# Kernel tuning notes

Hardware: AMD Instinct MI355X
Metric: run time of the kernel (lower is better)

## Reference

```python
import jax, jax.numpy as jnp
import numpy as np

B, S = 2048, 256
V, E, H, LAT, NL = 4, 8, 64, 3, 2
NT = V + 2          # vocab + start + pad tokens
START = V
TEMP = 1.0


def setup_inputs() -> dict:
    key = jax.random.key(0)
    ks = jax.random.split(key, 32)
    def p(k, shape, scale=0.1):
        return jax.random.normal(k, shape, jnp.float32) * scale
    return {
        "tokens": jax.random.randint(ks[0], (B, S), 0, V),
        "emb": p(ks[1], (NT, E)),
        "enc_Wih0": p(ks[2], (3 * H, E)), "enc_Whh0": p(ks[3], (3 * H, H)),
        "enc_bih0": p(ks[4], (3 * H,)), "enc_bhh0": p(ks[5], (3 * H,)),
        "enc_Wih1": p(ks[6], (3 * H, H)), "enc_Whh1": p(ks[7], (3 * H, H)),
        "enc_bih1": p(ks[8], (3 * H,)), "enc_bhh1": p(ks[9], (3 * H,)),
        "fc_mu_W": p(ks[10], (LAT, H)), "fc_mu_b": p(ks[11], (LAT,)),
        "fc_var_W": p(ks[12], (LAT, H)), "fc_var_b": p(ks[13], (LAT,)),
        "dec_emb": p(ks[14], (NT, H)),
        "proj_W": p(ks[15], (H, LAT)), "proj_b": p(ks[16], (H,)),
        "dec_Wih0": p(ks[17], (3 * H, H)), "dec_Whh0": p(ks[18], (3 * H, H)),
        "dec_bih0": p(ks[19], (3 * H,)), "dec_bhh0": p(ks[20], (3 * H,)),
        "dec_Wih1": p(ks[21], (3 * H, H)), "dec_Whh1": p(ks[22], (3 * H, H)),
        "dec_bih1": p(ks[23], (3 * H,)), "dec_bhh1": p(ks[24], (3 * H,)),
        "head_W": p(ks[25], (V, H)), "head_b": p(ks[26], (V,)),
    }


def gru_cell(h, x, Wih, Whh, bih, bhh):
    # PyTorch GRU gate order: reset, update, new
    gi = x @ Wih.T + bih            # [B, 3H]
    gh = h @ Whh.T + bhh            # [B, 3H]
    ir, iz, ig = jnp.split(gi, 3, axis=-1)
    hr, hz, hg = jnp.split(gh, 3, axis=-1)
    r = jax.nn.sigmoid(ir + hr)
    z = jax.nn.sigmoid(iz + hz)
    n = jnp.tanh(ig + r * hg)
    return (1.0 - z) * n + z * h


def run_gru_layer(x, Wih, Whh, bih, bhh):
    # x: [B, S, D] -> (outputs [B, S, H], final hidden [B, H])
    def step(h, xt):
        h2 = gru_cell(h, xt, Wih, Whh, bih, bhh)
        return h2, h2
    h0 = jnp.zeros((x.shape[0], Whh.shape[1]), x.dtype)
    hT, ys = jax.lax.scan(step, h0, x.transpose(1, 0, 2))
    return ys.transpose(1, 0, 2), hT


def reference(tokens, emb, enc_Wih0, enc_Whh0, enc_bih0, enc_bhh0,
              enc_Wih1, enc_Whh1, enc_bih1, enc_bhh1,
              fc_mu_W, fc_mu_b, fc_var_W, fc_var_b,
              dec_emb, proj_W, proj_b,
              dec_Wih0, dec_Whh0, dec_bih0, dec_bhh0,
              dec_Wih1, dec_Whh1, dec_bih1, dec_bhh1,
              head_W, head_b):
    b, s = tokens.shape
    # ---- encode ----
    x = emb[tokens]                                   # [B, S, E]
    seq, _ = run_gru_layer(x, enc_Wih0, enc_Whh0, enc_bih0, enc_bhh0)
    _, h_last = run_gru_layer(seq, enc_Wih1, enc_Whh1, enc_bih1, enc_bhh1)
    mu = h_last @ fc_mu_W.T + fc_mu_b                 # [B, LAT]
    log_var = h_last @ fc_var_W.T + fc_var_b          # [B, LAT]
    # ---- reparameterize ----
    eps = jax.random.normal(jax.random.key(1), mu.shape, mu.dtype)
    z = eps * jnp.exp(0.5 * log_var) + mu
    hz = z @ proj_W.T + proj_b                        # [B, H]; same init for both layers
    tok0 = jnp.full((b,), START, jnp.int32)
    keys = jax.random.split(jax.random.key(2), s)
    def step(carry, k):
        h0, h1, tok = carry
        xe = dec_emb[tok]                             # [B, H]
        h0n = gru_cell(h0, xe, dec_Wih0, dec_Whh0, dec_bih0, dec_bhh0)
        h1n = gru_cell(h1, h0n, dec_Wih1, dec_Whh1, dec_bih1, dec_bhh1)
        logits = (h1n @ head_W.T + head_b) / TEMP     # [B, V]
        probs = jax.nn.softmax(logits, axis=-1)
        nt = jax.random.categorical(k, logits)        # multinomial sample (detached)
        return (h0n, h1n, nt), probs
    _, probs_seq = jax.lax.scan(step, (hz, hz, tok0), keys)   # [S, B, V]
    recons = probs_seq.transpose(1, 0, 2)[:, :, None, :]      # [B, S, 1, V]
    return recons, tokens, mu, log_var
```

## Files before the change

### kernel.cpp

```cpp
#include <hip/hip_runtime.h>
#include <stdint.h>

typedef unsigned int u32;

#define NB   2048
#define SS   256
#define HH   64
#define VV   4
#define LATD 3
#define NTHR 512

#define TOK_OFF (NB*SS*VV)
#define MU_OFF  (TOK_OFF + NB*SS)
#define LV_OFF  (MU_OFF + NB*LATD)

__device__ __forceinline__ void tf2x32(u32 k0, u32 k1, u32 x0, u32 x1, u32& o0, u32& o1){
  u32 k2 = k0 ^ k1 ^ 0x1BD11BDAu;
  x0 += k0; x1 += k1;
#define TFR(r) { x0 += x1; x1 = (x1<<r)|(x1>>(32-r)); x1 ^= x0; }
  TFR(13) TFR(15) TFR(26) TFR(6)   x0 += k1; x1 += k2 + 1u;
  TFR(17) TFR(29) TFR(16) TFR(24)  x0 += k2; x1 += k0 + 2u;
  TFR(13) TFR(15) TFR(26) TFR(6)   x0 += k0; x1 += k1 + 3u;
  TFR(17) TFR(29) TFR(16) TFR(24)  x0 += k1; x1 += k2 + 4u;
  TFR(13) TFR(15) TFR(26) TFR(6)   x0 += k2; x1 += k0 + 5u;
#undef TFR
  o0 = x0; o1 = x1;
}
__device__ __forceinline__ u32 foldb(u32 k0, u32 k1, u32 i){
  u32 a,b; tf2x32(k0,k1,0u,i,a,b); return a^b;
}
__device__ __forceinline__ float b2u(u32 bits){
  union{u32 i;float f;}c; c.i = (bits>>9) | 0x3f800000u; return c.f - 1.0f;
}
__device__ __forceinline__ float erfinv_f(float x){
  float w = -log1pf(-x*x);
  float p;
  if (w < 5.0f){
    w -= 2.5f;
    p = 2.81022636e-08f;
    p = fmaf(p,w, 3.43273939e-07f);
    p = fmaf(p,w,-3.5233877e-06f);
    p = fmaf(p,w,-4.39150654e-06f);
    p = fmaf(p,w, 0.00021858087f);
    p = fmaf(p,w,-0.00125372503f);
    p = fmaf(p,w,-0.00417768164f);
    p = fmaf(p,w, 0.246640727f);
    p = fmaf(p,w, 1.50140941f);
  } else {
    w = sqrtf(w) - 3.0f;
    p = -0.000200214257f;
    p = fmaf(p,w, 0.000100950558f);
    p = fmaf(p,w, 0.00134934322f);
    p = fmaf(p,w,-0.00367342844f);
    p = fmaf(p,w, 0.00573950773f);
    p = fmaf(p,w,-0.0076224613f);
    p = fmaf(p,w, 0.00943887047f);
    p = fmaf(p,w, 1.00167406f);
    p = fmaf(p,w, 2.83297682f);
  }
  return p*x;
}
__device__ __forceinline__ float sigm(float x){ return 1.0f/(1.0f+expf(-x)); }
__device__ __forceinline__ float rl(float x, int l){
  return __int_as_float(__builtin_amdgcn_readlane(__float_as_int(x), l));
}
__device__ __forceinline__ float wred(float x){
  #pragma unroll
  for (int m=1; m<64; m<<=1) x += __shfl_xor(x, m, 64);
  return x;
}

#define PIN4(v) asm volatile("" : "+v"(v.x), "+v"(v.y), "+v"(v.z), "+v"(v.w))
#define PIN_W8(Ar, Az, An)                                                     \
  _Pragma("unroll")                                                            \
  for (int k4 = 0; k4 < 8; k4++){ PIN4(Ar[k4]); PIN4(An[k4]); PIN4(Az[k4]); }

#define MATVEC0P(hA, hB)                                                       \
  _Pragma("unroll")                                                            \
  for (int k4 = 0; k4 < 8; k4++){                                              \
    float4 wr = w0r[k4], wz = w0z[k4], wn = w0n[k4];                           \
    int kb = kb0 + 4*k4;                                                       \
    float a0=rl(hA,kb), a1=rl(hA,kb+1), a2=rl(hA,kb+2), a3=rl(hA,kb+3);        \
    float c0=rl(hB,kb), c1=rl(hB,kb+1), c2=rl(hB,kb+2), c3=rl(hB,kb+3);        \
    arA=fmaf(wr.x,a0,arA); arA=fmaf(wr.y,a1,arA); arA=fmaf(wr.z,a2,arA); arA=fmaf(wr.w,a3,arA); \
    azA=fmaf(wz.x,a0,azA); azA=fmaf(wz.y,a1,azA); azA=fmaf(wz.z,a2,azA); azA=fmaf(wz.w,a3,azA); \
    anA=fmaf(wn.x,a0,anA); anA=fmaf(wn.y,a1,anA); anA=fmaf(wn.z,a2,anA); anA=fmaf(wn.w,a3,anA); \
    arB=fmaf(wr.x,c0,arB); arB=fmaf(wr.y,c1,arB); arB=fmaf(wr.z,c2,arB); arB=fmaf(wr.w,c3,arB); \
    azB=fmaf(wz.x,c0,azB); azB=fmaf(wz.y,c1,azB); azB=fmaf(wz.z,c2,azB); azB=fmaf(wz.w,c3,azB); \
    anB=fmaf(wn.x,c0,anB); anB=fmaf(wn.y,c1,anB); anB=fmaf(wn.z,c2,anB); anB=fmaf(wn.w,c3,anB); \
  }

#define MATVEC1P(xA, xB, yA, yB)                                               \
  _Pragma("unroll 2")                                                          \
  for (int k4 = 0; k4 < 8; k4++){                                              \
    int ki = kh8 + k4;                                                         \
    float4 wir = wi1[ki*192 + j],  wiz = wi1[ki*192 + 64 + j],  win = wi1[ki*192 + 128 + j]; \
    float4 whr = wh1[ki*192 + j],  whz = wh1[ki*192 + 64 + j],  whn = wh1[ki*192 + 128 + j]; \
    int kb = 4*ki;                                                             \
    float xa0=rl(xA,kb), xa1=rl(xA,kb+1), xa2=rl(xA,kb+2), xa3=rl(xA,kb+3);    \
    float xb0=rl(xB,kb), xb1=rl(xB,kb+1), xb2=rl(xB,kb+2), xb3=rl(xB,kb+3);    \
    float ya0=rl(yA,kb), ya1=rl(yA,kb+1), ya2=rl(yA,kb+2), ya3=rl(yA,kb+3);    \
    float yb0=rl(yB,kb), yb1=rl(yB,kb+1), yb2=rl(yB,kb+2), yb3=rl(yB,kb+3);    \
    srA=fmaf(wir.x,xa0,srA); srA=fmaf(wir.y,xa1,srA); srA=fmaf(wir.z,xa2,srA); srA=fmaf(wir.w,xa3,srA); \
    srA=fmaf(whr.x,ya0,srA); srA=fmaf(whr.y,ya1,srA); srA=fmaf(whr.z,ya2,srA); srA=fmaf(whr.w,ya3,srA); \
    szA=fmaf(wiz.x,xa0,szA); szA=fmaf(wiz.y,xa1,szA); szA=fmaf(wiz.z,xa2,szA); szA=fmaf(wiz.w,xa3,szA); \
    szA=fmaf(whz.x,ya0,szA); szA=fmaf(whz.y,ya1,szA); szA=fmaf(whz.z,ya2,szA); szA=fmaf(whz.w,ya3,szA); \
    inA=fmaf(win.x,xa0,inA); inA=fmaf(win.y,xa1,inA); inA=fmaf(win.z,xa2,inA); inA=fmaf(win.w,xa3,inA); \
    hnA=fmaf(whn.x,ya0,hnA); hnA=fmaf(whn.y,ya1,hnA); hnA=fmaf(whn.z,ya2,hnA); hnA=fmaf(whn.w,ya3,hnA); \
    srB=fmaf(wir.x,xb0,srB); srB=fmaf(wir.y,xb1,srB); srB=fmaf(wir.z,xb2,srB); srB=fmaf(wir.w,xb3,srB); \
    srB=fmaf(whr.x,yb0,srB); srB=fmaf(whr.y,yb1,srB); srB=fmaf(whr.z,yb2,srB); srB=fmaf(whr.w,yb3,srB); \
    szB=fmaf(wiz.x,xb0,szB); szB=fmaf(wiz.y,xb1,szB); szB=fmaf(wiz.z,xb2,szB); szB=fmaf(wiz.w,xb3,szB); \
    szB=fmaf(whz.x,yb0,szB); szB=fmaf(whz.y,yb1,szB); szB=fmaf(whz.z,yb2,szB); szB=fmaf(whz.w,yb3,szB); \
    inB=fmaf(win.x,xb0,inB); inB=fmaf(win.y,xb1,inB); inB=fmaf(win.z,xb2,inB); inB=fmaf(win.w,xb3,inB); \
    hnB=fmaf(whn.x,yb0,hnB); hnB=fmaf(whn.y,yb1,hnB); hnB=fmaf(whn.z,yb2,hnB); hnB=fmaf(whn.w,yb3,hnB); \
  }

__global__ __launch_bounds__(NTHR, 2) void enc_kernel(
    const int* __restrict__ tokens, const float* __restrict__ emb,
    const float* __restrict__ Wih0, const float* __restrict__ Whh0,
    const float* __restrict__ bih0, const float* __restrict__ bhh0,
    const float* __restrict__ Wih1, const float* __restrict__ Whh1,
    const float* __restrict__ bih1, const float* __restrict__ bhh1,
    const float* __restrict__ muW, const float* __restrict__ mub,
    const float* __restrict__ vaW, const float* __restrict__ vab,
    const float* __restrict__ pW,  const float* __restrict__ pb,
    float* __restrict__ out, float* __restrict__ hz_ws)
{
  __shared__ float4 wi1[16*192];
  __shared__ float4 wh1[16*192];
  __shared__ float tokT[VV*192];
  __shared__ float4 ex1a[8][64];
  __shared__ float2 ex1b[8][64];
  __shared__ float4 ex2a[8][64];
  __shared__ float4 ex2b[8][64];

  const int tid = threadIdx.x;
  const int b0  = blockIdx.x * 8;
  const int j   = tid & 63;
  const int wv  = tid >> 6;
  const int kh  = wv & 1;
  const int pw  = wv ^ 1;
  const int rA  = b0 + (wv & ~1);
  const int rB  = rA + 1;
  const int rD  = b0 + wv;
  const int kh8 = kh * 8;
  const int kb0 = kh * 32;

  for (int i4 = tid; i4 < 3072; i4 += NTHR){
    int g = i4 >> 4, k4 = i4 & 15;
    wi1[k4*192 + g] = ((const float4*)Wih1)[i4];
    wh1[k4*192 + g] = ((const float4*)Whh1)[i4];
  }
  if (tid < 192){
    #pragma unroll
    for (int v = 0; v < VV; v++){
      float acc = 0.0f;
      #pragma unroll
      for (int e = 0; e < 8; e++) acc = fmaf(emb[v*8+e], Wih0[tid*8+e], acc);
      tokT[v*192 + tid] = acc + bih0[tid];
    }
  }
  for (int i = tid; i < 8*SS; i += NTHR){
    int rr = i >> 8, tq = i & 255;
    out[TOK_OFF + (b0+rr)*SS + tq] = (float)tokens[(b0+rr)*SS + tq];
  }

  float4 w0r[8], w0z[8], w0n[8];
  {
    const float4* G0 = (const float4*)Whh0;
    #pragma unroll
    for (int k4 = 0; k4 < 8; k4++){
      w0r[k4] = G0[(j)*16      + kh8 + k4];
      w0z[k4] = G0[(64 + j)*16 + kh8 + k4];
      w0n[k4] = G0[(128 + j)*16+ kh8 + k4];
    }
    PIN_W8(w0r, w0z, w0n)
  }
  __syncthreads();

  const float bhr0 = bhh0[j], bhz0 = bhh0[64+j], bhn0 = bhh0[128+j];
  const float bR1  = bih1[j]      + bhh1[j];
  const float bZ1  = bih1[64+j]   + bhh1[64+j];
  const float bin1 = bih1[128+j], bhn1 = bhh1[128+j];

  float h0A = 0.0f, h0B = 0.0f, h1A = 0.0f, h1B = 0.0f;

  for (int t = 0; t < SS; t++){
    asm volatile("" ::: "memory");
    int kA = tokens[rA*SS + t];
    int kB = tokens[rB*SS + t];
    float arA=0, azA=0, anA=0, arB=0, azB=0, anB=0;
    MATVEC0P(h0A, h0B)
    ex1a[wv][j] = make_float4(arA, azA, anA, arB);
    ex1b[wv][j] = make_float2(azB, anB);
    __syncthreads();
    {
      float4 qa = ex1a[pw][j]; float2 qb = ex1b[pw][j];
      arA += qa.x; azA += qa.y; anA += qa.z;
      arB += qa.w; azB += qb.x; anB += qb.y;
    }
    {
      float ir = tokT[kA*192+j], iz = tokT[kA*192+64+j], ig = tokT[kA*192+128+j];
      float rg = sigm(ir + arA + bhr0);
      float zg = sigm(iz + azA + bhz0);
      float ng = tanhf(ig + rg*(anA + bhn0));
      h0A = (1.0f - zg)*ng + zg*h0A;
    }
    {
      float ir = tokT[kB*192+j], iz = tokT[kB*192+64+j], ig = tokT[kB*192+128+j];
      float rg = sigm(ir + arB + bhr0);
      float zg = sigm(iz + azB + bhz0);
      float ng = tanhf(ig + rg*(anB + bhn0));
      h0B = (1.0f - zg)*ng + zg*h0B;
    }
    float srA=0, szA=0, inA=0, hnA=0, srB=0, szB=0, inB=0, hnB=0;
    MATVEC1P(h0A, h0B, h1A, h1B)
    ex2a[wv][j] = make_float4(srA, szA, inA, hnA);
    ex2b[wv][j] = make_float4(srB, szB, inB, hnB);
    __syncthreads();
    {
      float4 pa = ex2a[pw][j];
      float rg = sigm(srA + pa.x + bR1);
      float zg = sigm(szA + pa.y + bZ1);
      float ng = tanhf(inA + pa.z + bin1 + rg*(hnA + pa.w + bhn1));
      h1A = (1.0f - zg)*ng + zg*h1A;
      float4 pb = ex2b[pw][j];
      rg = sigm(srB + pb.x + bR1);
      zg = sigm(szB + pb.y + bZ1);
      ng = tanhf(inB + pb.z + bin1 + rg*(hnB + pb.w + bhn1));
      h1B = (1.0f - zg)*ng + zg*h1B;
    }
  }

  const float LO_ = -0.99999994f;
  {
    float hv = kh ? h1B : h1A;
    int gb = rD;
    float mu0,mu1,mu2, lv0,lv1,lv2;
    { float pm = muW[0*64+j]*hv; pm = wred(pm); mu0 = pm + mub[0];
      float pv = vaW[0*64+j]*hv; pv = wred(pv); lv0 = pv + vab[0]; }
    { float pm = muW[1*64+j]*hv; pm = wred(pm); mu1 = pm + mub[1];
      float pv = vaW[1*64+j]*hv; pv = wred(pv); lv1 = pv + vab[1]; }
    { float pm = muW[2*64+j]*hv; pm = wred(pm); mu2 = pm + mub[2];
      float pv = vaW[2*64+j]*hv; pv = wred(pv); lv2 = pv + vab[2]; }
    if (j < 3){
      float mv  = (j==0)?mu0:(j==1)?mu1:mu2;
      float lvv = (j==0)?lv0:(j==1)?lv1:lv2;
      out[MU_OFF + gb*LATD + j] = mv;
      out[LV_OFF + gb*LATD + j] = lvv;
    }
    float z0,z1,z2;
    #pragma unroll
    for (int l = 0; l < 3; l++){
      u32 bits = foldb(0u, 1u, (u32)(gb*LATD + l));
      float u01 = b2u(bits);
      float uu = u01 * 2.0f;
      uu = uu + LO_;
      uu = fmaxf(LO_, uu);
      float ep = 1.41421354f * erfinv_f(uu);
      float lvv = (l==0)?lv0:(l==1)?lv1:lv2;
      float mvv = (l==0)?mu0:(l==1)?mu1:mu2;
      float zv = ep * expf(0.5f*lvv) + mvv;
      if (l==0) z0 = zv; else if (l==1) z1 = zv; else z2 = zv;
    }
    float hzj = pW[j*3+0]*z0;
    hzj += pW[j*3+1]*z1;
    hzj += pW[j*3+2]*z2;
    hzj += pb[j];
    hz_ws[gb*HH + j] = hzj;
  }
}

__global__ __launch_bounds__(NTHR, 2) void dec_kernel(
    const float* __restrict__ demb,
    const float* __restrict__ Wih0, const float* __restrict__ Whh0,
    const float* __restrict__ bih0, const float* __restrict__ bhh0,
    const float* __restrict__ Wih1, const float* __restrict__ Whh1,
    const float* __restrict__ bih1, const float* __restrict__ bhh1,
    const float* __restrict__ headW, const float* __restrict__ headb,
    const float* __restrict__ hz_ws, float* __restrict__ out)
{
  __shared__ float4 wi1[16*192];
  __shared__ float4 wh1[16*192];
  __shared__ float decT[6*192];
  __shared__ u32 sk0[SS], sk1[SS];
  __shared__ int tokS[8];
  __shared__ float4 ex1a[8][64];
  __shared__ float2 ex1b[8][64];
  __shared__ float4 ex2a[8][64];
  __shared__ float4 ex2b[8][64];

  const int tid = threadIdx.x;
  const int b0  = blockIdx.x * 8;
  const int j   = tid & 63;
  const int wv  = tid >> 6;
  const int kh  = wv & 1;
  const int pw  = wv ^ 1;
  const int rA  = b0 + (wv & ~1);
  const int rB  = rA + 1;
  const int rD  = b0 + wv;
  const int kh8 = kh * 8;
  const int kb0 = kh * 32;
  const int pbase = wv & ~1;

  for (int i4 = tid; i4 < 3072; i4 += NTHR){
    int g = i4 >> 4, k4 = i4 & 15;
    wi1[k4*192 + g] = ((const float4*)Wih1)[i4];
    wh1[k4*192 + g] = ((const float4*)Whh1)[i4];
  }
  if (tid < 192){
    #pragma unroll
    for (int v = 0; v < 6; v++){
      float acc = 0.0f;
      #pragma unroll 8
      for (int k = 0; k < 64; k++) acc = fmaf(demb[v*64+k], Wih0[tid*64+k], acc);
      decT[v*192 + tid] = acc + bih0[tid];
    }
  }
  if (tid < SS){
    u32 a,b; tf2x32(0u, 2u, 0u, (u32)tid, a, b);
    sk0[tid] = a; sk1[tid] = b;
  }
  if (tid < 8) tokS[tid] = 4;

  float4 w0r[8], w0z[8], w0n[8];
  {
    const float4* G0 = (const float4*)Whh0;
    #pragma unroll
    for (int k4 = 0; k4 < 8; k4++){
      w0r[k4] = G0[(j)*16      + kh8 + k4];
      w0z[k4] = G0[(64 + j)*16 + kh8 + k4];
      w0n[k4] = G0[(128 + j)*16+ kh8 + k4];
    }
    PIN_W8(w0r, w0z, w0n)
  }
  __syncthreads();

  const float bhr0 = bhh0[j], bhz0 = bhh0[64+j], bhn0 = bhh0[128+j];
  const float bR1  = bih1[j]      + bhh1[j];
  const float bZ1  = bih1[64+j]   + bhh1[64+j];
  const float bin1 = bih1[128+j], bhn1 = bhh1[128+j];
  const float hw0 = headW[0*64+j], hw1 = headW[1*64+j], hw2 = headW[2*64+j], hw3 = headW[3*64+j];
  const float hb0 = headb[0], hb1 = headb[1], hb2 = headb[2], hb3 = headb[3];

  float h0A = hz_ws[rA*HH + j];
  float h0B = hz_ws[rB*HH + j];
  float h1A = h0A, h1B = h0B;

  const int vv = j & 3;
  const float TINY = 1.17549435e-38f;

  for (int t = 0; t < SS; t++){
    asm volatile("" ::: "memory");
    float arA=0, azA=0, anA=0, arB=0, azB=0, anB=0;
    MATVEC0P(h0A, h0B)
    ex1a[wv][j] = make_float4(arA, azA, anA, arB);
    ex1b[wv][j] = make_float2(azB, anB);
    __syncthreads();
    int tkA = tokS[pbase];
    int tkB = tokS[pbase+1];
    {
      float4 qa = ex1a[pw][j]; float2 qb = ex1b[pw][j];
      arA += qa.x; azA += qa.y; anA += qa.z;
      arB += qa.w; azB += qb.x; anB += qb.y;
    }
    {
      float ir = decT[tkA*192+j], iz = decT[tkA*192+64+j], ig = decT[tkA*192+128+j];
      float rg = sigm(ir + arA + bhr0);
      float zg = sigm(iz + azA + bhz0);
      float ng = tanhf(ig + rg*(anA + bhn0));
      h0A = (1.0f - zg)*ng + zg*h0A;
    }
    {
      float ir = decT[tkB*192+j], iz = decT[tkB*192+64+j], ig = decT[tkB*192+128+j];
      float rg = sigm(ir + arB + bhr0);
      float zg = sigm(iz + azB + bhz0);
      float ng = tanhf(ig + rg*(anB + bhn0));
      h0B = (1.0f - zg)*ng + zg*h0B;
    }
    float srA=0, szA=0, inA=0, hnA=0, srB=0, szB=0, inB=0, hnB=0;
    MATVEC1P(h0A, h0B, h1A, h1B)
    ex2a[wv][j] = make_float4(srA, szA, inA, hnA);
    ex2b[wv][j] = make_float4(srB, szB, inB, hnB);
    __syncthreads();
    {
      float4 pa = ex2a[pw][j];
      float rg = sigm(srA + pa.x + bR1);
      float zg = sigm(szA + pa.y + bZ1);
      float ng = tanhf(inA + pa.z + bin1 + rg*(hnA + pa.w + bhn1));
      h1A = (1.0f - zg)*ng + zg*h1A;
      float4 pb = ex2b[pw][j];
      rg = sigm(srB + pb.x + bR1);
      zg = sigm(szB + pb.y + bZ1);
      ng = tanhf(inB + pb.z + bin1 + rg*(hnB + pb.w + bhn1));
      h1B = (1.0f - zg)*ng + zg*h1B;
    }
    float hD = kh ? h1B : h1A;
    float l0 = wred(hw0*hD) + hb0;
    float l1 = wred(hw1*hD) + hb1;
    float l2 = wred(hw2*hD) + hb2;
    float l3 = wred(hw3*hD) + hb3;
    float lg = (vv==0)?l0:(vv==1)?l1:(vv==2)?l2:l3;
    u32 bits = foldb(sk0[t], sk1[t], (u32)(rD*VV + vv));
    float u01 = b2u(bits);
    float u = u01 + TINY;
    u = fmaxf(TINY, u);
    float gmb = -logf(-logf(u));
    float prt = lg + gmb;
    float mx = lg;
    mx = fmaxf(mx, __shfl_xor(mx, 1, 64));
    mx = fmaxf(mx, __shfl_xor(mx, 2, 64));
    float e = expf(lg - mx);
    float se = e;
    se += __shfl_xor(se, 1, 64);
    se += __shfl_xor(se, 2, 64);
    float prob = e / se;
    float bp = prt; int bv = vv;
    { float o = __shfl_xor(bp, 1, 64); int ov = __shfl_xor(bv, 1, 64);
      if (o > bp || (o == bp && ov < bv)){ bp = o; bv = ov; } }
    { float o = __shfl_xor(bp, 2, 64); int ov = __shfl_xor(bv, 2, 64);
      if (o > bp || (o == bp && ov < bv)){ bp = o; bv = ov; } }
    if (j < 4) out[(size_t)rD*SS*VV + (size_t)t*VV + vv] = prob;
    int tkD = __builtin_amdgcn_readlane(bv, 0);
    if (j == 0) tokS[wv] = tkD;
  }
}

extern "C" void kernel_launch(void* const* d_in, const int* in_sizes, int n_in,
                              void* d_out, int out_size, void* d_ws, size_t ws_size,
                              hipStream_t stream){
  const int*   tokens = (const int*)d_in[0];
  const float* emb    = (const float*)d_in[1];
  const float* eWih0  = (const float*)d_in[2];  const float* eWhh0 = (const float*)d_in[3];
  const float* ebih0  = (const float*)d_in[4];  const float* ebhh0 = (const float*)d_in[5];
  const float* eWih1  = (const float*)d_in[6];  const float* eWhh1 = (const float*)d_in[7];
  const float* ebih1  = (const float*)d_in[8];  const float* ebhh1 = (const float*)d_in[9];
  const float* muW    = (const float*)d_in[10]; const float* mub   = (const float*)d_in[11];
  const float* vaW    = (const float*)d_in[12]; const float* vab   = (const float*)d_in[13];
  const float* demb   = (const float*)d_in[14];
  const float* pW     = (const float*)d_in[15]; const float* pb    = (const float*)d_in[16];
  const float* dWih0  = (const float*)d_in[17]; const float* dWhh0 = (const float*)d_in[18];
  const float* dbih0  = (const float*)d_in[19]; const float* dbhh0 = (const float*)d_in[20];
  const float* dWih1  = (const float*)d_in[21]; const float* dWhh1 = (const float*)d_in[22];
  const float* dbih1  = (const float*)d_in[23]; const float* dbhh1 = (const float*)d_in[24];
  const float* hWp    = (const float*)d_in[25]; const float* hbp   = (const float*)d_in[26];
  float* out = (float*)d_out;
  float* hz = (float*)d_ws;

  enc_kernel<<<NB/8, NTHR, 0, stream>>>(tokens, emb,
      eWih0, eWhh0, ebih0, ebhh0, eWih1, eWhh1, ebih1, ebhh1,
      muW, mub, vaW, vab, pW, pb, out, hz);
  dec_kernel<<<NB/8, NTHR, 0, stream>>>(demb,
      dWih0, dWhh0, dbih0, dbhh0, dWih1, dWhh1, dbih1, dbhh1,
      hWp, hbp, hz, out);
}
```

Baseline: 2.928 ms.

## Drop K-split across wave pairs; each wave does full matvec for two rows

Each wave now computes the full 64-wide recurrent matvecs for its two batch rows, keeping all of Whh0 in registers (48 float4) instead of splitting K across a wave pair. This removes the shared-memory partial-sum exchange and both block-wide barriers per timestep, and keeps sampled tokens in registers. In exchange, blocks shrink to 256 threads with 1 block per SIMD-occupancy target, register pressure doubles, and each wave does twice the FMA and readlane work serially.

```diff
diff --git a/kernel.cpp b/kernel.cpp
--- a/kernel.cpp
+++ b/kernel.cpp
@@ -8,7 +8,7 @@
 #define HH   64
 #define VV   4
 #define LATD 3
-#define NTHR 512
+#define NTHR 256
 
 #define TOK_OFF (NB*SS*VV)
 #define MU_OFF  (TOK_OFF + NB*SS)
@@ -71,15 +71,23 @@
 }
 
 #define PIN4(v) asm volatile("" : "+v"(v.x), "+v"(v.y), "+v"(v.z), "+v"(v.w))
-#define PIN_W8(Ar, Az, An)                                                     \
+#define PIN_W(Ar, Az, An)                                                      \
   _Pragma("unroll")                                                            \
-  for (int k4 = 0; k4 < 8; k4++){ PIN4(Ar[k4]); PIN4(An[k4]); PIN4(Az[k4]); }
-
-#define MATVEC0P(hA, hB)                                                       \
+  for (int k4 = 0; k4 < 16; k4++){ PIN4(Ar[k4]); PIN4(An[k4]); PIN4(Az[k4]); }
+
+#define LOAD_REG_W(G, Ar, Az, An)                                              \
   _Pragma("unroll")                                                            \
-  for (int k4 = 0; k4 < 8; k4++){                                              \
+  for (int k4 = 0; k4 < 16; k4++){                                             \
+    Ar[k4] = G[(j)*16 + k4];                                                   \
+    Az[k4] = G[(64 + j)*16 + k4];                                              \
+    An[k4] = G[(128 + j)*16 + k4];                                             \
+  }
+
+#define MATVEC0F(hA, hB)                                                       \
+  _Pragma("unroll")                                                            \
+  for (int k4 = 0; k4 < 16; k4++){                                             \
     float4 wr = w0r[k4], wz = w0z[k4], wn = w0n[k4];                           \
-    int kb = kb0 + 4*k4;                                                       \
+    int kb = 4*k4;                                                             \
     float a0=rl(hA,kb), a1=rl(hA,kb+1), a2=rl(hA,kb+2), a3=rl(hA,kb+3);        \
     float c0=rl(hB,kb), c1=rl(hB,kb+1), c2=rl(hB,kb+2), c3=rl(hB,kb+3);        \
     arA=fmaf(wr.x,a0,arA); arA=fmaf(wr.y,a1,arA); arA=fmaf(wr.z,a2,arA); arA=fmaf(wr.w,a3,arA); \
@@ -90,17 +98,16 @@
     anB=fmaf(wn.x,c0,anB); anB=fmaf(wn.y,c1,anB); anB=fmaf(wn.z,c2,anB); anB=fmaf(wn.w,c3,anB); \
   }
 
-#define MATVEC1P(xA, xB, yA, yB)                                               \
+#define MATVEC1F                                                               \
   _Pragma("unroll 2")                                                          \
-  for (int k4 = 0; k4 < 8; k4++){                                              \
-    int ki = kh8 + k4;                                                         \
-    float4 wir = wi1[ki*192 + j],  wiz = wi1[ki*192 + 64 + j],  win = wi1[ki*192 + 128 + j]; \
-    float4 whr = wh1[ki*192 + j],  whz = wh1[ki*192 + 64 + j],  whn = wh1[ki*192 + 128 + j]; \
-    int kb = 4*ki;                                                             \
-    float xa0=rl(xA,kb), xa1=rl(xA,kb+1), xa2=rl(xA,kb+2), xa3=rl(xA,kb+3);    \
-    float xb0=rl(xB,kb), xb1=rl(xB,kb+1), xb2=rl(xB,kb+2), xb3=rl(xB,kb+3);    \
-    float ya0=rl(yA,kb), ya1=rl(yA,kb+1), ya2=rl(yA,kb+2), ya3=rl(yA,kb+3);    \
-    float yb0=rl(yB,kb), yb1=rl(yB,kb+1), yb2=rl(yB,kb+2), yb3=rl(yB,kb+3);    \
+  for (int k4 = 0; k4 < 16; k4++){                                             \
+    float4 wir = wi1[k4*192 + j],  wiz = wi1[k4*192 + 64 + j],  win = wi1[k4*192 + 128 + j]; \
+    float4 whr = wh1[k4*192 + j],  whz = wh1[k4*192 + 64 + j],  whn = wh1[k4*192 + 128 + j]; \
+    int kb = 4*k4;                                                             \
+    float xa0=rl(h0A,kb), xa1=rl(h0A,kb+1), xa2=rl(h0A,kb+2), xa3=rl(h0A,kb+3); \
+    float xb0=rl(h0B,kb), xb1=rl(h0B,kb+1), xb2=rl(h0B,kb+2), xb3=rl(h0B,kb+3); \
+    float ya0=rl(h1A,kb), ya1=rl(h1A,kb+1), ya2=rl(h1A,kb+2), ya3=rl(h1A,kb+3); \
+    float yb0=rl(h1B,kb), yb1=rl(h1B,kb+1), yb2=rl(h1B,kb+2), yb3=rl(h1B,kb+3); \
     srA=fmaf(wir.x,xa0,srA); srA=fmaf(wir.y,xa1,srA); srA=fmaf(wir.z,xa2,srA); srA=fmaf(wir.w,xa3,srA); \
     srA=fmaf(whr.x,ya0,srA); srA=fmaf(whr.y,ya1,srA); srA=fmaf(whr.z,ya2,srA); srA=fmaf(whr.w,ya3,srA); \
     szA=fmaf(wiz.x,xa0,szA); szA=fmaf(wiz.y,xa1,szA); szA=fmaf(wiz.z,xa2,szA); szA=fmaf(wiz.w,xa3,szA); \
@@ -115,7 +122,7 @@
     hnB=fmaf(whn.x,yb0,hnB); hnB=fmaf(whn.y,yb1,hnB); hnB=fmaf(whn.z,yb2,hnB); hnB=fmaf(whn.w,yb3,hnB); \
   }
 
-__global__ __launch_bounds__(NTHR, 2) void enc_kernel(
+__global__ __launch_bounds__(NTHR, 1) void enc_kernel(
     const int* __restrict__ tokens, const float* __restrict__ emb,
     const float* __restrict__ Wih0, const float* __restrict__ Whh0,
     const float* __restrict__ bih0, const float* __restrict__ bhh0,
@@ -129,22 +136,13 @@
   __shared__ float4 wi1[16*192];
   __shared__ float4 wh1[16*192];
   __shared__ float tokT[VV*192];
-  __shared__ float4 ex1a[8][64];
-  __shared__ float2 ex1b[8][64];
-  __shared__ float4 ex2a[8][64];
-  __shared__ float4 ex2b[8][64];
 
   const int tid = threadIdx.x;
   const int b0  = blockIdx.x * 8;
   const int j   = tid & 63;
   const int wv  = tid >> 6;
-  const int kh  = wv & 1;
-  const int pw  = wv ^ 1;
-  const int rA  = b0 + (wv & ~1);
+  const int rA  = b0 + 2*wv;
   const int rB  = rA + 1;
-  const int rD  = b0 + wv;
-  const int kh8 = kh * 8;
-  const int kb0 = kh * 32;
 
   for (int i4 = tid; i4 < 3072; i4 += NTHR){
     int g = i4 >> 4, k4 = i4 & 15;
@@ -165,16 +163,11 @@
     out[TOK_OFF + (b0+rr)*SS + tq] = (float)tokens[(b0+rr)*SS + tq];
   }
 
-  float4 w0r[8], w0z[8], w0n[8];
+  float4 w0r[16], w0z[16], w0n[16];
   {
     const float4* G0 = (const float4*)Whh0;
-    #pragma unroll
-    for (int k4 = 0; k4 < 8; k4++){
-      w0r[k4] = G0[(j)*16      + kh8 + k4];
-      w0z[k4] = G0[(64 + j)*16 + kh8 + k4];
-      w0n[k4] = G0[(128 + j)*16+ kh8 + k4];
-    }
-    PIN_W8(w0r, w0z, w0n)
+    LOAD_REG_W(G0, w0r, w0z, w0n)
+    PIN_W(w0r, w0z, w0n)
   }
   __syncthreads();
 
@@ -190,15 +183,7 @@
     int kA = tokens[rA*SS + t];
     int kB = tokens[rB*SS + t];
     float arA=0, azA=0, anA=0, arB=0, azB=0, anB=0;
-    MATVEC0P(h0A, h0B)
-    ex1a[wv][j] = make_float4(arA, azA, anA, arB);
-    ex1b[wv][j] = make_float2(azB, anB);
-    __syncthreads();
-    {
-      float4 qa = ex1a[pw][j]; float2 qb = ex1b[pw][j];
-      arA += qa.x; azA += qa.y; anA += qa.z;
-      arB += qa.w; azB += qb.x; anB += qb.y;
-    }
+    MATVEC0F(h0A, h0B)
     {
       float ir = tokT[kA*192+j], iz = tokT[kA*192+64+j], ig = tokT[kA*192+128+j];
       float rg = sigm(ir + arA + bhr0);
@@ -214,28 +199,24 @@
       h0B = (1.0f - zg)*ng + zg*h0B;
     }
     float srA=0, szA=0, inA=0, hnA=0, srB=0, szB=0, inB=0, hnB=0;
-    MATVEC1P(h0A, h0B, h1A, h1B)
-    ex2a[wv][j] = make_float4(srA, szA, inA, hnA);
-    ex2b[wv][j] = make_float4(srB, szB, inB, hnB);
-    __syncthreads();
-    {
-      float4 pa = ex2a[pw][j];
-      float rg = sigm(srA + pa.x + bR1);
-      float zg = sigm(szA + pa.y + bZ1);
-      float ng = tanhf(inA + pa.z + bin1 + rg*(hnA + pa.w + bhn1));
+    MATVEC1F
+    {
+      float rg = sigm(srA + bR1);
+      float zg = sigm(szA + bZ1);
+      float ng = tanhf(inA + bin1 + rg*(hnA + bhn1));
       h1A = (1.0f - zg)*ng + zg*h1A;
-      float4 pb = ex2b[pw][j];
-      rg = sigm(srB + pb.x + bR1);
-      zg = sigm(szB + pb.y + bZ1);
-      ng = tanhf(inB + pb.z + bin1 + rg*(hnB + pb.w + bhn1));
+      rg = sigm(srB + bR1);
+      zg = sigm(szB + bZ1);
+      ng = tanhf(inB + bin1 + rg*(hnB + bhn1));
       h1B = (1.0f - zg)*ng + zg*h1B;
     }
   }
 
   const float LO_ = -0.99999994f;
-  {
-    float hv = kh ? h1B : h1A;
-    int gb = rD;
+  #pragma unroll
+  for (int rr = 0; rr < 2; rr++){
+    float hv = rr ? h1B : h1A;
+    int gb = rr ? rB : rA;
     float mu0,mu1,mu2, lv0,lv1,lv2;
     { float pm = muW[0*64+j]*hv; pm = wred(pm); mu0 = pm + mub[0];
       float pv = vaW[0*64+j]*hv; pv = wred(pv); lv0 = pv + vab[0]; }
@@ -271,7 +252,7 @@
   }
 }
 
-__global__ __launch_bounds__(NTHR, 2) void dec_kernel(
+__global__ __launch_bounds__(NTHR, 1) void dec_kernel(
     const float* __restrict__ demb,
     const float* __restrict__ Wih0, const float* __restrict__ Whh0,
     const float* __restrict__ bih0, const float* __restrict__ bhh0,
@@ -284,24 +265,13 @@
   __shared__ float4 wh1[16*192];
   __shared__ float decT[6*192];
   __shared__ u32 sk0[SS], sk1[SS];
-  __shared__ int tokS[8];
-  __shared__ float4 ex1a[8][64];
-  __shared__ float2 ex1b[8][64];
-  __shared__ float4 ex2a[8][64];
-  __shared__ float4 ex2b[8][64];
 
   const int tid = threadIdx.x;
   const int b0  = blockIdx.x * 8;
   const int j   = tid & 63;
   const int wv  = tid >> 6;
-  const int kh  = wv & 1;
-  const int pw  = wv ^ 1;
-  const int rA  = b0 + (wv & ~1);
+  const int rA  = b0 + 2*wv;
   const int rB  = rA + 1;
-  const int rD  = b0 + wv;
-  const int kh8 = kh * 8;
-  const int kb0 = kh * 32;
-  const int pbase = wv & ~1;
 
   for (int i4 = tid; i4 < 3072; i4 += NTHR){
     int g = i4 >> 4, k4 = i4 & 15;
@@ -321,18 +291,12 @@
     u32 a,b; tf2x32(0u, 2u, 0u, (u32)tid, a, b);
     sk0[tid] = a; sk1[tid] = b;
   }
-  if (tid < 8) tokS[tid] = 4;
-
-  float4 w0r[8], w0z[8], w0n[8];
+
+  float4 w0r[16], w0z[16], w0n[16];
   {
     const float4* G0 = (const float4*)Whh0;
-    #pragma unroll
-    for (int k4 = 0; k4 < 8; k4++){
-      w0r[k4] = G0[(j)*16      + kh8 + k4];
-      w0z[k4] = G0[(64 + j)*16 + kh8 + k4];
-      w0n[k4] = G0[(128 + j)*16+ kh8 + k4];
-    }
-    PIN_W8(w0r, w0z, w0n)
+    LOAD_REG_W(G0, w0r, w0z, w0n)
+    PIN_W(w0r, w0z, w0n)
   }
   __syncthreads();
 
@@ -346,6 +310,7 @@
   float h0A = hz_ws[rA*HH + j];
   float h0B = hz_ws[rB*HH + j];
   float h1A = h0A, h1B = h0B;
+  int tkA = 4, tkB = 4;
 
   const int vv = j & 3;
   const float TINY = 1.17549435e-38f;
@@ -353,17 +318,7 @@
   for (int t = 0; t < SS; t++){
     asm volatile("" ::: "memory");
     float arA=0, azA=0, anA=0, arB=0, azB=0, anB=0;
-    MATVEC0P(h0A, h0B)
-    ex1a[wv][j] = make_float4(arA, azA, anA, arB);
-    ex1b[wv][j] = make_float2(azB, anB);
-    __syncthreads();
-    int tkA = tokS[pbase];
-    int tkB = tokS[pbase+1];
-    {
-      float4 qa = ex1a[pw][j]; float2 qb = ex1b[pw][j];
-      arA += qa.x; azA += qa.y; anA += qa.z;
-      arB += qa.w; azB += qb.x; anB += qb.y;
-    }
+    MATVEC0F(h0A, h0B)
     {
       float ir = decT[tkA*192+j], iz = decT[tkA*192+64+j], ig = decT[tkA*192+128+j];
       float rg = sigm(ir + arA + bhr0);
@@ -379,50 +334,49 @@
       h0B = (1.0f - zg)*ng + zg*h0B;
     }
     float srA=0, szA=0, inA=0, hnA=0, srB=0, szB=0, inB=0, hnB=0;
-    MATVEC1P(h0A, h0B, h1A, h1B)
-    ex2a[wv][j] = make_float4(srA, szA, inA, hnA);
-    ex2b[wv][j] = make_float4(srB, szB, inB, hnB);
-    __syncthreads();
-    {
-      float4 pa = ex2a[pw][j];
-      float rg = sigm(srA + pa.x + bR1);
-      float zg = sigm(szA + pa.y + bZ1);
-      float ng = tanhf(inA + pa.z + bin1 + rg*(hnA + pa.w + bhn1));
+    MATVEC1F
+    {
+      float rg = sigm(srA + bR1);
+      float zg = sigm(szA + bZ1);
+      float ng = tanhf(inA + bin1 + rg*(hnA + bhn1));
       h1A = (1.0f - zg)*ng + zg*h1A;
-      float4 pb = ex2b[pw][j];
-      rg = sigm(srB + pb.x + bR1);
-      zg = sigm(szB + pb.y + bZ1);
-      ng = tanhf(inB + pb.z + bin1 + rg*(hnB + pb.w + bhn1));
+      rg = sigm(srB + bR1);
+      zg = sigm(szB + bZ1);
+      ng = tanhf(inB + bin1 + rg*(hnB + bhn1));
       h1B = (1.0f - zg)*ng + zg*h1B;
     }
-    float hD = kh ? h1B : h1A;
-    float l0 = wred(hw0*hD) + hb0;
-    float l1 = wred(hw1*hD) + hb1;
-    float l2 = wred(hw2*hD) + hb2;
-    float l3 = wred(hw3*hD) + hb3;
-    float lg = (vv==0)?l0:(vv==1)?l1:(vv==2)?l2:l3;
-    u32 bits = foldb(sk0[t], sk1[t], (u32)(rD*VV + vv));
-    float u01 = b2u(bits);
-    float u = u01 + TINY;
-    u = fmaxf(TINY, u);
-    float gmb = -logf(-logf(u));
-    float prt = lg + gmb;
-    float mx = lg;
-    mx = fmaxf(mx, __shfl_xor(mx, 1, 64));
-    mx = fmaxf(mx, __shfl_xor(mx, 2, 64));
-    float e = expf(lg - mx);
-    float se = e;
-    se += __shfl_xor(se, 1, 64);
-    se += __shfl_xor(se, 2, 64);
-    float prob = e / se;
-    float bp = prt; int bv = vv;
-    { float o = __shfl_xor(bp, 1, 64); int ov = __shfl_xor(bv, 1, 64);
-      if (o > bp || (o == bp && ov < bv)){ bp = o; bv = ov; } }
-    { float o = __shfl_xor(bp, 2, 64); int ov = __shfl_xor(bv, 2, 64);
-      if (o > bp || (o == bp && ov < bv)){ bp = o; bv = ov; } }
-    if (j < 4) out[(size_t)rD*SS*VV + (size_t)t*VV + vv] = prob;
-    int tkD = __builtin_amdgcn_readlane(bv, 0);
-    if (j == 0) tokS[wv] = tkD;
+    #pragma unroll
+    for (int rr = 0; rr < 2; rr++){
+      float hD = rr ? h1B : h1A;
+      int gb = rr ? rB : rA;
+      float l0 = wred(hw0*hD) + hb0;
+      float l1 = wred(hw1*hD) + hb1;
+      float l2 = wred(hw2*hD) + hb2;
+      float l3 = wred(hw3*hD) + hb3;
+      float lg = (vv==0)?l0:(vv==1)?l1:(vv==2)?l2:l3;
+      u32 bits = foldb(sk0[t], sk1[t], (u32)(gb*VV + vv));
+      float u01 = b2u(bits);
+      float u = u01 + TINY;
+      u = fmaxf(TINY, u);
+      float gmb = -logf(-logf(u));
+      float prt = lg + gmb;
+      float mx = lg;
+      mx = fmaxf(mx, __shfl_xor(mx, 1, 64));
+      mx = fmaxf(mx, __shfl_xor(mx, 2, 64));
+      float e = expf(lg - mx);
+      float se = e;
+      se += __shfl_xor(se, 1, 64);
+      se += __shfl_xor(se, 2, 64);
+      float prob = e / se;
+      float bp = prt; int bv = vv;
+      { float o = __shfl_xor(bp, 1, 64); int ov = __shfl_xor(bv, 1, 64);
+        if (o > bp || (o == bp && ov < bv)){ bp = o; bv = ov; } }
+      { float o = __shfl_xor(bp, 2, 64); int ov = __shfl_xor(bv, 2, 64);
+        if (o > bp || (o == bp && ov < bv)){ bp = o; bv = ov; } }
+      if (j < 4) out[(size_t)gb*SS*VV + (size_t)t*VV + vv] = prob;
+      int tkD = __builtin_amdgcn_readlane(bv, 0);
+      if (rr == 0) tkA = tkD; else tkB = tkD;
+    }
   }
 }
 
```

After: 3.322 ms. +13.5%, slower.
